# Optimization experiments

Measured on AMD Instinct MI355X. Metric: run time of the kernel, lower is better.

The kernel has to match this reference:

```python
import jax, jax.numpy as jnp
import numpy as np

WINDOW_SIZE = 11
SIGMA = 1.5

def _gaussian_window():
    x = np.arange(WINDOW_SIZE, dtype=np.float64) - WINDOW_SIZE // 2
    g = np.exp(-(x ** 2) / (2.0 * SIGMA ** 2))
    g = (g / g.sum()).astype(np.float32)
    w2 = np.outer(g, g)  # [11, 11]
    return jnp.asarray(w2)


def setup_inputs() -> dict:
    key = jax.random.key(0)
    k1, k2 = jax.random.split(key)
    B, C, H, W = 32, 3, 512, 512
    img1 = jax.random.uniform(k1, (B, C, H, W), dtype=jnp.float32)
    img2 = jax.random.uniform(k2, (B, C, H, W), dtype=jnp.float32)
    return {"img1": img1, "img2": img2}


def reference(img1, img2):
    # peak = 1.0, size_average = True
    c1 = jnp.float32(0.01 ** 2)
    c2 = jnp.float32(0.03 ** 2)
    C = img1.shape[1]
    w2 = _gaussian_window()

    # One fused depthwise conv over the 5 statistic planes (same math as 5
    # separate grouped convs in the original).
    stacked = jnp.concatenate(
        [img1, img2, img1 * img1, img2 * img2, img1 * img2], axis=1
    )  # [B, 5C, H, W]
    kernel = jnp.tile(w2[None, None], (5 * C, 1, 1, 1))  # [5C, 1, 11, 11]
    out = jax.lax.conv_general_dilated(
        stacked, kernel,
        window_strides=(1, 1), padding='VALID',
        feature_group_count=5 * C,
        dimension_numbers=('NCHW', 'OIHW', 'NCHW'),
    )  # [B, 5C, H-10, W-10]

    mu1 = out[:, 0 * C:1 * C]
    mu2 = out[:, 1 * C:2 * C]
    mu1_sq = mu1 * mu1
    mu2_sq = mu2 * mu2
    mu1_mu2 = mu1 * mu2
    sigma1_sq = out[:, 2 * C:3 * C] - mu1_sq
    sigma2_sq = out[:, 3 * C:4 * C] - mu2_sq
    sigma12 = out[:, 4 * C:5 * C] - mu1_mu2

    ssim_map = ((2 * mu1_mu2 + c1) * (2 * sigma12 + c2)) / (
        (mu1_sq + mu2_sq + c1) * (sigma1_sq + sigma2_sq + c2)
    )
    return jnp.mean(ssim_map)
```

## Files before the change

### kernel.cpp

```cpp
#include <hip/hip_runtime.h>


namespace {
constexpr int IMG_H = 512;
constexpr int IMG_W = 512;
constexpr int NIMG  = 96;
constexpr int OUT_H = 502;
constexpr int OUT_W = 502;
constexpr int RPB   = 24;
constexpr int QR    = 2;
constexpr int WIN   = QR + 10;
constexpr int BUFW  = 544;
constexpr double TOTAL = 24192384.0;

constexpr double U0 = 0.0038659201;
constexpr double U1 = 0.0285655007;
constexpr double U2 = 0.1353352832366127;
constexpr double U3 = 0.4111122898;
constexpr double U4 = 0.8007374026;
constexpr double S  = 1.0 + 2.0 * (U0 + U1 + U2 + U3 + U4);
}

typedef float vf2 __attribute__((ext_vector_type(2)));

__device__ __forceinline__ vf2 pk_fma(float w, vf2 a, vf2 c) {
    vf2 wv = {w, w};
    return __builtin_elementwise_fma(wv, a, c);
}

__global__ __launch_bounds__(256, 3) void ssim_main(const float* __restrict__ img1,
                                                    const float* __restrict__ img2,
                                                    double* __restrict__ acc)
{
    __shared__ __align__(16) float vrow[QR][4][BUFW];
    __shared__ float red[4];

    const float g[11] = {
        (float)(U0/S), (float)(U1/S), (float)(U2/S), (float)(U3/S), (float)(U4/S),
        (float)(1.0/S),
        (float)(U4/S), (float)(U3/S), (float)(U2/S), (float)(U1/S), (float)(U0/S)
    };
    constexpr float C1 = 1e-4f;
    constexpr float C2 = 9e-4f;

    const int t   = threadIdx.x;
    const int z   = blockIdx.y;
    const int oy0 = blockIdx.x * RPB;
    const int row_end = min(oy0 + RPB, OUT_H);

    const vf2* p1 = (const vf2*)(img1 + (size_t)z * (IMG_H * IMG_W)) + t;
    const vf2* p2 = (const vf2*)(img2 + (size_t)z * (IMG_H * IMG_W)) + t;

    const int c4w  = t >> 1;
    const int woff = ((c4w ^ ((c4w >> 3) & 7)) << 2) + ((t & 1) << 1);

    const int hq = t >> 7;
    const int cb = (t & 127) << 2;
    int roff[4];
    #pragma unroll
    for (int k = 0; k < 4; ++k) {
        int c4 = (cb >> 2) + k;
        roff[k] = (c4 ^ ((c4 >> 3) & 7)) << 2;
    }

    vf2 wx[WIN], wy[WIN];
    #pragma unroll
    for (int j = 0; j < WIN - QR; ++j) {
        wx[j] = p1[(oy0 + j) * (IMG_W / 2)];
        wy[j] = p2[(oy0 + j) * (IMG_W / 2)];
    }

    float local = 0.f;

    for (int r0 = oy0; r0 < row_end; r0 += QR) {
        #pragma unroll
        for (int i = 0; i < QR; ++i) {
            const int row = min(r0 + (WIN - QR) + i, IMG_H - 1);
            wx[WIN - QR + i] = p1[row * (IMG_W / 2)];
            wy[WIN - QR + i] = p2[row * (IMG_W / 2)];
        }

        vf2 am1[QR], am2[QR], app[QR], axy[QR];
        #pragma unroll
        for (int q = 0; q < QR; ++q) {
            am1[q] = (vf2){0.f, 0.f};
            am2[q] = (vf2){0.f, 0.f};
            app[q] = (vf2){0.f, 0.f};
            axy[q] = (vf2){0.f, 0.f};
        }
        #pragma unroll
        for (int j = 0; j < WIN; ++j) {
            const vf2 x = wx[j], y = wy[j];
            const vf2 pp = __builtin_elementwise_fma(y, y, x * x);
            const vf2 xy = x * y;
            #pragma unroll
            for (int q = 0; q < QR; ++q) {
                const int k = j - q;
                if (k >= 0 && k < 11) {
                    const float w = g[k];
                    am1[q] = pk_fma(w, x,  am1[q]);
                    am2[q] = pk_fma(w, y,  am2[q]);
                    app[q] = pk_fma(w, pp, app[q]);
                    axy[q] = pk_fma(w, xy, axy[q]);
                }
            }
        }
        __syncthreads();
        #pragma unroll
        for (int q = 0; q < QR; ++q) {
            *(vf2*)&vrow[q][0][woff] = am1[q];
            *(vf2*)&vrow[q][1][woff] = am2[q];
            *(vf2*)&vrow[q][2][woff] = app[q];
            *(vf2*)&vrow[q][3][woff] = axy[q];
        }
        __syncthreads();

        #pragma unroll
        for (int j = 0; j < WIN - QR; ++j) { wx[j] = wx[j + QR]; wy[j] = wy[j + QR]; }

        const int rr = r0 + hq;
        if (rr < row_end && cb < OUT_W) {
            float aa[4][4];
            #pragma unroll
            for (int ch = 0; ch < 4; ++ch) {
                const float* bc = &vrow[hq][ch][0];
                float f[16];
                #pragma unroll
                for (int k = 0; k < 4; ++k) {
                    float4 v = *(const float4*)(bc + roff[k]);
                    f[4*k+0] = v.x; f[4*k+1] = v.y; f[4*k+2] = v.z; f[4*k+3] = v.w;
                }
                #pragma unroll
                for (int j = 0; j < 4; ++j) {
                    float s = 0.f;
                    #pragma unroll
                    for (int k = 0; k < 11; ++k) s = fmaf(g[k], f[j + k], s);
                    aa[ch][j] = s;
                }
            }
            #pragma unroll
            for (int j = 0; j < 4; ++j) {
                if (cb + j < OUT_W) {
                    float mu1 = aa[0][j], mu2 = aa[1][j];
                    float ee  = aa[2][j], e12 = aa[3][j];
                    float mu11 = mu1 * mu1;
                    float mu22 = mu2 * mu2;
                    float mu12 = mu1 * mu2;
                    float mm   = mu11 + mu22;
                    float s12  = e12 - mu12;
                    float spp  = ee - mm;
                    float num = fmaf(2.f, mu12, C1) * fmaf(2.f, s12, C2);
                    float den = (mm + C1) * (spp + C2);
                    local = fmaf(num, __builtin_amdgcn_rcpf(den), local);
                }
            }
        }
    }

    #pragma unroll
    for (int off = 32; off > 0; off >>= 1) local += __shfl_down(local, off, 64);
    if ((t & 63) == 0) red[t >> 6] = local;
    __syncthreads();
    if (t == 0) {
        double s = (double)red[0] + (double)red[1] + (double)red[2] + (double)red[3];
        atomicAdd(acc, s);
    }
}

__global__ void ssim_fin(const double* __restrict__ acc, float* __restrict__ out)
{
    out[0] = (float)(acc[0] / TOTAL);
}

extern "C" void kernel_launch(void* const* d_in, const int* in_sizes, int n_in,
                              void* d_out, int out_size, void* d_ws, size_t ws_size,
                              hipStream_t stream)
{
    (void)in_sizes; (void)n_in; (void)out_size; (void)ws_size;
    const float* img1 = (const float*)d_in[0];
    const float* img2 = (const float*)d_in[1];
    double* acc = (double*)d_ws;

    hipMemsetAsync(d_ws, 0, sizeof(double), stream);
    dim3 grid((OUT_H + RPB - 1) / RPB, NIMG);
    hipLaunchKernelGGL(ssim_main, grid, dim3(256), 0, stream, img1, img2, acc);
    hipLaunchKernelGGL(ssim_fin, dim3(1), dim3(1), 0, stream, acc, (float*)d_out);
}
```

Baseline: 240.1 us.

## Interleave vertical sums in LDS for packed horizontal FMA and ring-buffer rows

Vertical-pass results are now stored in LDS as interleaved pairs (mu1/mu2 and pp/xy per column), so the horizontal 11-tap pass can use packed two-wide FMAs on two channels at once with fewer, wider LDS reads. The row loop is fully unrolled and the sliding row window becomes a modular ring buffer, which removes the register shifts each iteration. Launch bounds drop from 3 to 2 blocks per CU, which gives more registers to the unrolled code at the cost of occupancy.

```diff
diff --git a/kernel.cpp b/kernel.cpp
--- a/kernel.cpp
+++ b/kernel.cpp
@@ -10,7 +10,7 @@
 constexpr int RPB   = 24;
 constexpr int QR    = 2;
 constexpr int WIN   = QR + 10;
-constexpr int BUFW  = 544;
+constexpr int NQ    = 272;
 constexpr double TOTAL = 24192384.0;
 
 constexpr double U0 = 0.0038659201;
@@ -22,17 +22,19 @@
 }
 
 typedef float vf2 __attribute__((ext_vector_type(2)));
+typedef float vf4 __attribute__((ext_vector_type(4)));
 
 __device__ __forceinline__ vf2 pk_fma(float w, vf2 a, vf2 c) {
     vf2 wv = {w, w};
     return __builtin_elementwise_fma(wv, a, c);
 }
 
-__global__ __launch_bounds__(256, 3) void ssim_main(const float* __restrict__ img1,
+__global__ __launch_bounds__(256, 2) void ssim_main(const float* __restrict__ img1,
                                                     const float* __restrict__ img2,
                                                     double* __restrict__ acc)
 {
-    __shared__ __align__(16) float vrow[QR][4][BUFW];
+    __shared__ __align__(16) float ldsA[QR][NQ * 4];
+    __shared__ __align__(16) float ldsB[QR][NQ * 4];
     __shared__ float red[4];
 
     const float g[11] = {
@@ -51,16 +53,16 @@
     const vf2* p1 = (const vf2*)(img1 + (size_t)z * (IMG_H * IMG_W)) + t;
     const vf2* p2 = (const vf2*)(img2 + (size_t)z * (IMG_H * IMG_W)) + t;
 
-    const int c4w  = t >> 1;
-    const int woff = ((c4w ^ ((c4w >> 3) & 7)) << 2) + ((t & 1) << 1);
+    const int woff = (t ^ ((t >> 3) & 7)) << 2;
 
     const int hq = t >> 7;
     const int cb = (t & 127) << 2;
-    int roff[4];
-    #pragma unroll
-    for (int k = 0; k < 4; ++k) {
-        int c4 = (cb >> 2) + k;
-        roff[k] = (c4 ^ ((c4 >> 3) & 7)) << 2;
+    const int qb = (t & 127) << 1;
+    int roff[7];
+    #pragma unroll
+    for (int m = 0; m < 7; ++m) {
+        const int q = qb + m;
+        roff[m] = (q ^ ((q >> 3) & 7)) << 2;
     }
 
     vf2 wx[WIN], wy[WIN];
@@ -72,12 +74,17 @@
 
     float local = 0.f;
 
-    for (int r0 = oy0; r0 < row_end; r0 += QR) {
+    #pragma unroll
+    for (int u = 0; u < RPB / QR; ++u) {
+        const int r0 = oy0 + u * QR;
+        if (r0 >= row_end) break;
+
         #pragma unroll
         for (int i = 0; i < QR; ++i) {
-            const int row = min(r0 + (WIN - QR) + i, IMG_H - 1);
-            wx[WIN - QR + i] = p1[row * (IMG_W / 2)];
-            wy[WIN - QR + i] = p2[row * (IMG_W / 2)];
+            const int slot = (2 * u + 10 + i) % WIN;
+            const int row  = min(r0 + 10 + i, IMG_H - 1);
+            wx[slot] = p1[row * (IMG_W / 2)];
+            wy[slot] = p2[row * (IMG_W / 2)];
         }
 
         vf2 am1[QR], am2[QR], app[QR], axy[QR];
@@ -90,7 +97,8 @@
         }
         #pragma unroll
         for (int j = 0; j < WIN; ++j) {
-            const vf2 x = wx[j], y = wy[j];
+            const int slot = (2 * u + j) % WIN;
+            const vf2 x = wx[slot], y = wy[slot];
             const vf2 pp = __builtin_elementwise_fma(y, y, x * x);
             const vf2 xy = x * y;
             #pragma unroll
@@ -108,49 +116,60 @@
         __syncthreads();
         #pragma unroll
         for (int q = 0; q < QR; ++q) {
-            *(vf2*)&vrow[q][0][woff] = am1[q];
-            *(vf2*)&vrow[q][1][woff] = am2[q];
-            *(vf2*)&vrow[q][2][woff] = app[q];
-            *(vf2*)&vrow[q][3][woff] = axy[q];
+            vf4 qa = {am1[q].x, am2[q].x, am1[q].y, am2[q].y};
+            vf4 qbv = {app[q].x, axy[q].x, app[q].y, axy[q].y};
+            *(vf4*)&ldsA[q][woff] = qa;
+            *(vf4*)&ldsB[q][woff] = qbv;
         }
         __syncthreads();
 
-        #pragma unroll
-        for (int j = 0; j < WIN - QR; ++j) { wx[j] = wx[j + QR]; wy[j] = wy[j + QR]; }
-
-        const int rr = r0 + hq;
-        if (rr < row_end && cb < OUT_W) {
-            float aa[4][4];
-            #pragma unroll
-            for (int ch = 0; ch < 4; ++ch) {
-                const float* bc = &vrow[hq][ch][0];
-                float f[16];
-                #pragma unroll
-                for (int k = 0; k < 4; ++k) {
-                    float4 v = *(const float4*)(bc + roff[k]);
-                    f[4*k+0] = v.x; f[4*k+1] = v.y; f[4*k+2] = v.z; f[4*k+3] = v.w;
-                }
+        if (r0 + hq < row_end && cb < OUT_W) {
+            vf2 sA[4], sB[4];
+            {
+                vf4 fq[7];
+                #pragma unroll
+                for (int m = 0; m < 7; ++m) fq[m] = *(const vf4*)&ldsA[hq][roff[m]];
                 #pragma unroll
                 for (int j = 0; j < 4; ++j) {
-                    float s = 0.f;
+                    vf2 s = (vf2){0.f, 0.f};
                     #pragma unroll
-                    for (int k = 0; k < 11; ++k) s = fmaf(g[k], f[j + k], s);
-                    aa[ch][j] = s;
+                    for (int k = 0; k < 11; ++k) {
+                        const int c = j + k;
+                        const vf2 f = (c & 1) ? fq[c >> 1].zw : fq[c >> 1].xy;
+                        s = pk_fma(g[k], f, s);
+                    }
+                    sA[j] = s;
+                }
+            }
+            {
+                vf4 fq[7];
+                #pragma unroll
+                for (int m = 0; m < 7; ++m) fq[m] = *(const vf4*)&ldsB[hq][roff[m]];
+                #pragma unroll
+                for (int j = 0; j < 4; ++j) {
+                    vf2 s = (vf2){0.f, 0.f};
+                    #pragma unroll
+                    for (int k = 0; k < 11; ++k) {
+                        const int c = j + k;
+                        const vf2 f = (c & 1) ? fq[c >> 1].zw : fq[c >> 1].xy;
+                        s = pk_fma(g[k], f, s);
+                    }
+                    sB[j] = s;
                 }
             }
             #pragma unroll
             for (int j = 0; j < 4; ++j) {
                 if (cb + j < OUT_W) {
-                    float mu1 = aa[0][j], mu2 = aa[1][j];
-                    float ee  = aa[2][j], e12 = aa[3][j];
-                    float mu11 = mu1 * mu1;
-                    float mu22 = mu2 * mu2;
-                    float mu12 = mu1 * mu2;
-                    float mm   = mu11 + mu22;
-                    float s12  = e12 - mu12;
-                    float spp  = ee - mm;
-                    float num = fmaf(2.f, mu12, C1) * fmaf(2.f, s12, C2);
-                    float den = (mm + C1) * (spp + C2);
+                    const float mu1 = sA[j].x, mu2 = sA[j].y;
+                    const float ee  = sB[j].x, e12 = sB[j].y;
+                    const float mu11 = mu1 * mu1;
+                    const float mu22 = mu2 * mu2;
+                    const float mu12 = mu1 * mu2;
+                    const float mm   = mu11 + mu22;
+                    const float s12  = e12 - mu12;
+                    const float spp  = ee - mm;
+                    const float num = fmaf(2.f, mu12, C1) * fmaf(2.f, s12, C2);
+                    const float den = (mm + C1) * (spp + C2);
                     local = fmaf(num, __builtin_amdgcn_rcpf(den), local);
                 }
             }
```

Result: slower. 247.0 us (+2.9%).
